# Performance work log

Measured on AMD Instinct MI355X. Metric: run time of the kernel, lower is better.

Reference implementation:

```python
import jax, jax.numpy as jnp
import numpy as np

N = 50000   # nodes
E = 800000  # edges
C = 64      # num_channels
EPS = 1e-5


def setup_inputs() -> dict:
    key = jax.random.key(0)
    ks = jax.random.split(key, 12)
    x = jax.random.normal(ks[0], (N, C), dtype=jnp.float32)
    vec = jax.random.normal(ks[1], (N, 3, C), dtype=jnp.float32)
    senders = jax.random.randint(ks[2], (E,), 0, N, dtype=jnp.int32)
    receivers = jax.random.randint(ks[3], (E,), 0, N, dtype=jnp.int32)
    interaction_matrices = jax.random.normal(ks[4], (E, 3, 3), dtype=jnp.float32)
    # learned parameters
    ln_scale = jnp.ones((C,), dtype=jnp.float32)
    ln_bias = jnp.zeros((C,), dtype=jnp.float32)
    vln_weight = jnp.ones((C,), dtype=jnp.float32)  # VecLayerNorm weight (norm_type='none' -> identity norm, channel scale)
    w1 = jax.random.normal(ks[5], (C, 2 * C), dtype=jnp.float32) / np.sqrt(C)
    b1 = jnp.zeros((2 * C,), dtype=jnp.float32)
    w2 = jax.random.normal(ks[6], (2 * C, C), dtype=jnp.float32) / np.sqrt(2 * C)
    b2 = jnp.zeros((C,), dtype=jnp.float32)
    return {
        "x": x, "vec": vec, "senders": senders, "receivers": receivers,
        "interaction_matrices": interaction_matrices,
        "ln_scale": ln_scale, "ln_bias": ln_bias, "vln_weight": vln_weight,
        "w1": w1, "b1": b1, "w2": w2, "b2": b2,
    }


def reference(x, vec, senders, receivers, interaction_matrices,
              ln_scale, ln_bias, vln_weight, w1, b1, w2, b2):
    # LayerNorm(eps=1e-5) over channel dim
    mean = jnp.mean(x, axis=-1, keepdims=True)
    var = jnp.var(x, axis=-1, keepdims=True)
    x_norm = (x - mean) * jax.lax.rsqrt(var + EPS) * ln_scale + ln_bias
    # VecLayerNorm with norm_type='none': identity norm, learned per-channel weight
    vec_norm = vec * vln_weight  # [N, 3, C]
    # MLP: Dense(2C) -> silu -> Dense(C)
    p = jax.nn.silu(x_norm @ w1 + b1) @ w2 + b2  # [N, C]
    # gather to edges
    p_i = p[receivers]            # [E, C]
    p_j = p[senders]              # [E, C]
    vec_i = vec_norm[receivers]   # [E, 3, C]
    vec_j = vec_norm[senders]     # [E, 3, C]
    source_dipole = p_j[:, None, :] * vec_j                              # [E, 3, C]
    field_at_i = jnp.einsum('eij,ejc->eic', interaction_matrices, source_dipole)  # [E, 3, C]
    dEnergy = jnp.sum(p_i[:, None, :] * vec_i * field_at_i, axis=1)      # [E, C]
    dx = jax.ops.segment_sum(dEnergy, receivers, num_segments=x.shape[0])  # [N, C]
    return dx
```

## Files before the change

### kernel.cpp

```cpp
#include <hip/hip_runtime.h>

#define C 64
#define EPS 1e-5f
#define BUCK_CAP 1536
#define OVF_CAP 65536
#define SMASK 0x03ffffffu

typedef __attribute__((ext_vector_type(8))) short bf16x8;
typedef __attribute__((ext_vector_type(4))) float f32x4;

static __device__ __forceinline__ unsigned int f2bf(float f) {
  unsigned int x = __float_as_uint(f);
  return (x + 0x7fffu + ((x >> 16) & 1u)) >> 16;
}
static __device__ __forceinline__ float bflo2f(unsigned int p) {
  return __uint_as_float(p << 16);
}
static __device__ __forceinline__ float bfhi2f(unsigned int p) {
  return __uint_as_float(p & 0xffff0000u);
}

__global__ __launch_bounds__(256) void prep_weights(
    const float* __restrict__ w1, const float* __restrict__ w2,
    unsigned short* __restrict__ w1T, unsigned short* __restrict__ w2T) {
  int idx = blockIdx.x * 256 + threadIdx.x;
  if (idx < 2 * C * C) {
    int k = idx >> 6, c = idx & 63;
    w1T[idx] = (unsigned short)f2bf(w1[c * 2 * C + k]);
  } else if (idx < 4 * C * C) {
    int j = idx - 2 * C * C;
    int c = j >> 7, k = j & 127;
    w2T[j] = (unsigned short)f2bf(w2[k * C + c]);
  }
}

__global__ __launch_bounds__(256) void bin_kernel(
    const int* __restrict__ recv, const int* __restrict__ send,
    uint2* __restrict__ region, int* __restrict__ bucketCnt,
    int* __restrict__ ovfList, int* __restrict__ ovfCnt,
    int n_edges, int nbuck) {
  __shared__ int hist[1024];
  int t = threadIdx.x;
  for (int i = t; i < 1024; i += 256) hist[i] = 0;
  __syncthreads();

  int base = blockIdx.x * 4096;
  int myrecv[16], mysend[16];
#pragma unroll 16
  for (int j = 0; j < 16; j++) {
    int e = base + j * 256 + t;
    if (e < n_edges) {
      int r = recv[e];
      myrecv[j] = r;
      mysend[j] = send[e];
      atomicAdd(&hist[r >> 6], 1);
    } else {
      myrecv[j] = -1;
      mysend[j] = 0;
    }
  }
  __syncthreads();

  for (int i = t; i < nbuck; i += 256) {
    int c = hist[i];
    hist[i] = (c > 0) ? atomicAdd(&bucketCnt[i], c) : 0;
  }
  __syncthreads();

#pragma unroll 16
  for (int j = 0; j < 16; j++) {
    int r = myrecv[j];
    if (r >= 0) {
      int e = base + j * 256 + t;
      int b = r >> 6;
      int pos = atomicAdd(&hist[b], 1);
      if (pos < BUCK_CAP) {
        uint2 rec;
        rec.x = (unsigned)mysend[j] | ((unsigned)(r & 63) << 26);
        rec.y = (unsigned)e;
        region[(size_t)b * BUCK_CAP + pos] = rec;
      } else {
        int o = atomicAdd(ovfCnt, 1);
        if (o < OVF_CAP) ovfList[o] = e;
      }
    }
  }
}

__global__ __launch_bounds__(256) void sort_kernel(
    uint2* __restrict__ region, const int* __restrict__ bucketCnt,
    int* __restrict__ nodeBeg, int* __restrict__ nodeEnd, int n_nodes) {
  __shared__ uint2 buf[BUCK_CAP];
  __shared__ int hist[64];
  __shared__ int off[64];
  int b = blockIdx.x;
  int t = threadIdx.x;
  int cnt = bucketCnt[b];
  if (cnt > BUCK_CAP) cnt = BUCK_CAP;
  uint2* reg = region + (size_t)b * BUCK_CAP;

  if (t < 64) hist[t] = 0;
  __syncthreads();
  for (int i = t; i < cnt; i += 256) {
    uint2 r = reg[i];
    buf[i] = r;
    atomicAdd(&hist[r.x >> 26], 1);
  }
  __syncthreads();
  if (t == 0) {
    int run = 0;
#pragma unroll
    for (int j = 0; j < 64; j++) { off[j] = run; run += hist[j]; }
  }
  __syncthreads();
  for (int i = t; i < cnt; i += 256) {
    uint2 r = buf[i];
    int pos = atomicAdd(&off[r.x >> 26], 1);
    reg[pos] = r;
  }
  __syncthreads();
  if (t < 64) {
    int node = b * 64 + t;
    if (node < n_nodes) {
      int end = off[t];
      nodeBeg[node] = b * BUCK_CAP + (end - hist[t]);
      nodeEnd[node] = b * BUCK_CAP + end;
    }
  }
}

__global__ __launch_bounds__(256, 4) void node_kernel(
    const float* __restrict__ x, const float* __restrict__ vec,
    const float* __restrict__ ln_scale, const float* __restrict__ ln_bias,
    const float* __restrict__ vln_w,
    const unsigned short* __restrict__ w1T, const float* __restrict__ b1,
    const unsigned short* __restrict__ w2T, const float* __restrict__ b2,
    uint2* __restrict__ D16, int n_nodes) {
  __shared__ unsigned short An[64 * 72];
  __shared__ unsigned short Ss[64 * 136];

  const int t = threadIdx.x;
  const int lane = t & 63;
  const int wave = t >> 6;
  const int l15 = lane & 15;
  const int q = lane >> 4;

  {
    int rowl = t >> 2;
    int part = t & 3;
    int node = blockIdx.x * 64 + rowl;
    int nc = node < n_nodes ? node : n_nodes - 1;
    const float* xp = x + (size_t)nc * C + part * 16;
    float xv[16];
    float s = 0.f;
#pragma unroll
    for (int i = 0; i < 4; i++) {
      float4 v = *(const float4*)(xp + i * 4);
      xv[i * 4 + 0] = v.x; xv[i * 4 + 1] = v.y;
      xv[i * 4 + 2] = v.z; xv[i * 4 + 3] = v.w;
      s += v.x + v.y + v.z + v.w;
    }
    s += __shfl_xor(s, 1);
    s += __shfl_xor(s, 2);
    float mean = s * (1.f / C);
    float vs = 0.f;
#pragma unroll
    for (int i = 0; i < 16; i++) {
      float d = xv[i] - mean;
      vs += d * d;
    }
    vs += __shfl_xor(vs, 1);
    vs += __shfl_xor(vs, 2);
    float rs = rsqrtf(vs * (1.f / C) + EPS);
    float ls[16], lb[16];
#pragma unroll
    for (int i = 0; i < 4; i++) {
      float4 a = *(const float4*)(ln_scale + part * 16 + i * 4);
      float4 b = *(const float4*)(ln_bias + part * 16 + i * 4);
      ls[i * 4 + 0] = a.x; ls[i * 4 + 1] = a.y; ls[i * 4 + 2] = a.z; ls[i * 4 + 3] = a.w;
      lb[i * 4 + 0] = b.x; lb[i * 4 + 1] = b.y; lb[i * 4 + 2] = b.z; lb[i * 4 + 3] = b.w;
    }
    unsigned int bp[8];
#pragma unroll
    for (int i = 0; i < 8; i++) {
      float e0 = (xv[2 * i] - mean) * rs * ls[2 * i] + lb[2 * i];
      float e1 = (xv[2 * i + 1] - mean) * rs * ls[2 * i + 1] + lb[2 * i + 1];
      bp[i] = f2bf(e0) | (f2bf(e1) << 16);
    }
    uint4* dst = (uint4*)(An + rowl * 72 + part * 16);
    uint4 p0 = {bp[0], bp[1], bp[2], bp[3]};
    uint4 p1 = {bp[4], bp[5], bp[6], bp[7]};
    dst[0] = p0;
    dst[1] = p1;
  }
  __syncthreads();

  const int Mbase = wave * 16;

  bf16x8 a0 = *(const bf16x8*)(An + (Mbase + l15) * 72 + q * 8);
  bf16x8 a1 = *(const bf16x8*)(An + (Mbase + l15) * 72 + 32 + q * 8);
  f32x4 acc1[8];
#pragma unroll
  for (int nt = 0; nt < 8; nt++) {
    const unsigned short* wb = w1T + (nt * 16 + l15) * 64 + q * 8;
    bf16x8 b0 = *(const bf16x8*)(wb);
    bf16x8 b1f = *(const bf16x8*)(wb + 32);
    f32x4 z = {0.f, 0.f, 0.f, 0.f};
    z = __builtin_amdgcn_mfma_f32_16x16x32_bf16(a0, b0, z, 0, 0, 0);
    z = __builtin_amdgcn_mfma_f32_16x16x32_bf16(a1, b1f, z, 0, 0, 0);
    acc1[nt] = z;
  }
#pragma unroll
  for (int nt = 0; nt < 8; nt++) {
    float bb = b1[nt * 16 + l15];
#pragma unroll
    for (int r = 0; r < 4; r++) {
      float h = acc1[nt][r] + bb;
      float sg = h / (1.f + __expf(-h));
      Ss[(Mbase + q * 4 + r) * 136 + nt * 16 + l15] = (unsigned short)f2bf(sg);
    }
  }
  __syncthreads();

  bf16x8 a2[4];
#pragma unroll
  for (int kt = 0; kt < 4; kt++)
    a2[kt] = *(const bf16x8*)(Ss + (Mbase + l15) * 136 + kt * 32 + q * 8);
  f32x4 acc2[4];
#pragma unroll
  for (int nt = 0; nt < 4; nt++) {
    f32x4 z = {0.f, 0.f, 0.f, 0.f};
#pragma unroll
    for (int kt = 0; kt < 4; kt++) {
      bf16x8 b = *(const bf16x8*)(w2T + (nt * 16 + l15) * 128 + kt * 32 + q * 8);
      z = __builtin_amdgcn_mfma_f32_16x16x32_bf16(a2[kt], b, z, 0, 0, 0);
    }
    acc2[nt] = z;
  }

#pragma unroll
  for (int nt = 0; nt < 4; nt++) {
    int cc = nt * 16 + l15;
    float bb = b2[cc];
    float vw = vln_w[cc];
#pragma unroll
    for (int r = 0; r < 4; r++) {
      int rl = Mbase + q * 4 + r;
      int nn = blockIdx.x * 64 + rl;
      if (nn < n_nodes) {
        float p = (acc2[nt][r] + bb) * vw;
        const float* vp = vec + (size_t)nn * (3 * C) + cc;
        float v0 = vp[0], v1 = vp[C], v2 = vp[2 * C];
        uint2 u;
        u.x = f2bf(p * v0) | (f2bf(p * v1) << 16);
        u.y = f2bf(p * v2);
        D16[(size_t)nn * C + cc] = u;
      }
    }
  }
}

__global__ __launch_bounds__(256) void accum_node(
    const uint2* __restrict__ region, const int* __restrict__ nodeBeg,
    const int* __restrict__ nodeEnd, const float* __restrict__ Mmat,
    const uint2* __restrict__ D2, float* __restrict__ dx, int n_nodes) {
  int wid = threadIdx.x >> 6;
  int lane = threadIdx.x & 63;
  int n = blockIdx.x * 4 + wid;
  if (n >= n_nodes) return;

  int beg = __builtin_amdgcn_readfirstlane(nodeBeg[n]);
  int end = __builtin_amdgcn_readfirstlane(nodeEnd[n]);

  uint2 dr = D2[(size_t)n * C + lane];
  float r0 = bflo2f(dr.x), r1 = bfhi2f(dr.x), r2 = bflo2f(dr.y);
  float acc = 0.f;

  if (beg < end) {
    const int last = end - 1;
    uint2 svA, svB, svC, svD, svE, svF;
    float mA[9], mB[9], mC[9], mD[9], mE[9], mF[9];

#define LOADSLOT(SV, MM, IDX)                                                \
  {                                                                          \
    uint2 rec_ = region[(IDX)];                                              \
    SV = D2[(size_t)(rec_.x & SMASK) * C + lane];                            \
    const float* Mp_ =                                                       \
        Mmat + (size_t)__builtin_amdgcn_readfirstlane((int)rec_.y) * 9;      \
    _Pragma("unroll") for (int j_ = 0; j_ < 9; j_++) MM[j_] = Mp_[j_];       \
  }

#define COMPUTE(SV, MM)                                                      \
  {                                                                          \
    float a0 = bflo2f(SV.x), a1 = bfhi2f(SV.x), a2 = bflo2f(SV.y);           \
    float f0 = MM[0] * a0 + MM[1] * a1 + MM[2] * a2;                         \
    float f1 = MM[3] * a0 + MM[4] * a1 + MM[5] * a2;                         \
    float f2 = MM[6] * a0 + MM[7] * a1 + MM[8] * a2;                         \
    acc += r0 * f0 + r1 * f1 + r2 * f2;                                      \
  }

    int i1 = (beg + 1 > last) ? last : beg + 1;
    int i2 = (beg + 2 > last) ? last : beg + 2;
    int i3 = (beg + 3 > last) ? last : beg + 3;
    int i4 = (beg + 4 > last) ? last : beg + 4;
    int i5 = (beg + 5 > last) ? last : beg + 5;
    LOADSLOT(svA, mA, beg)
    LOADSLOT(svB, mB, i1)
    LOADSLOT(svC, mC, i2)
    LOADSLOT(svD, mD, i3)
    LOADSLOT(svE, mE, i4)
    LOADSLOT(svF, mF, i5)

    for (int e = beg; e <= last; e += 6) {
#define STAGE(K, SV, MM)                                                     \
  if (e + (K) <= last) {                                                     \
    COMPUTE(SV, MM)                                                          \
    int nx = e + (K) + 6;                                                    \
    if (nx <= last) LOADSLOT(SV, MM, nx)                                     \
  }
      STAGE(0, svA, mA)
      STAGE(1, svB, mB)
      STAGE(2, svC, mC)
      STAGE(3, svD, mD)
      STAGE(4, svE, mE)
      STAGE(5, svF, mF)
#undef STAGE
    }
#undef LOADSLOT
#undef COMPUTE
  }
  dx[(size_t)n * C + lane] = acc;
}

__global__ __launch_bounds__(256) void fixup_kernel(
    const int* __restrict__ ovfList, const int* __restrict__ ovfCnt,
    const int* __restrict__ senders, const int* __restrict__ receivers,
    const float* __restrict__ Mmat, const uint2* __restrict__ D2,
    float* __restrict__ dx) {
  int nov = *ovfCnt;
  if (nov > OVF_CAP) nov = OVF_CAP;
  int lane = threadIdx.x & 63;
  for (int idx = blockIdx.x * 4 + (threadIdx.x >> 6); idx < nov;
       idx += gridDim.x * 4) {
    int e = ovfList[idx];
    int s = senders[e];
    int r = receivers[e];
    uint2 sv = D2[(size_t)s * C + lane];
    uint2 rv = D2[(size_t)r * C + lane];
    const float* M = Mmat + (size_t)e * 9;
    float a0 = bflo2f(sv.x), a1 = bfhi2f(sv.x), a2 = bflo2f(sv.y);
    float c0 = bflo2f(rv.x), c1 = bfhi2f(rv.x), c2 = bflo2f(rv.y);
    float f0 = M[0] * a0 + M[1] * a1 + M[2] * a2;
    float f1 = M[3] * a0 + M[4] * a1 + M[5] * a2;
    float f2 = M[6] * a0 + M[7] * a1 + M[8] * a2;
    float dE = c0 * f0 + c1 * f1 + c2 * f2;
    atomicAdd(dx + (size_t)r * C + lane, dE);
  }
}

extern "C" void kernel_launch(void* const* d_in, const int* in_sizes, int n_in,
                              void* d_out, int out_size, void* d_ws, size_t ws_size,
                              hipStream_t stream) {
  const float* x        = (const float*)d_in[0];
  const float* vec      = (const float*)d_in[1];
  const int*   senders  = (const int*)d_in[2];
  const int*   receivers= (const int*)d_in[3];
  const float* Mmat     = (const float*)d_in[4];
  const float* ln_scale = (const float*)d_in[5];
  const float* ln_bias  = (const float*)d_in[6];
  const float* vln_w    = (const float*)d_in[7];
  const float* w1       = (const float*)d_in[8];
  const float* b1       = (const float*)d_in[9];
  const float* w2       = (const float*)d_in[10];
  const float* b2       = (const float*)d_in[11];
  float* dx = (float*)d_out;

  int n_nodes = in_sizes[0] / C;
  int n_edges = in_sizes[2];
  int nbuck = (n_nodes + 63) >> 6;

  unsigned short* w1T = (unsigned short*)d_ws;
  unsigned short* w2T = w1T + 2 * C * C;
  uint2* D16 = (uint2*)((char*)d_ws + 32768);
  char* p = (char*)d_ws + 32768 + (size_t)n_nodes * C * sizeof(uint2);
  p = (char*)(((size_t)p + 255) & ~(size_t)255);
  int* cnts    = (int*)p;  p += (1024 + 1) * 4;
  p = (char*)(((size_t)p + 255) & ~(size_t)255);
  uint2* region = (uint2*)p;  p += (size_t)nbuck * BUCK_CAP * 8;
  int* nodeBeg = (int*)p;     p += (size_t)n_nodes * 4;
  int* nodeEnd = (int*)p;     p += (size_t)n_nodes * 4;
  int* ovfList = (int*)p;
  int* bucketCnt = cnts;
  int* ovfCnt = cnts + 1024;

  prep_weights<<<64, 256, 0, stream>>>(w1, w2, w1T, w2T);

  hipMemsetAsync(cnts, 0, (1024 + 1) * sizeof(int), stream);
  bin_kernel<<<(n_edges + 4095) / 4096, 256, 0, stream>>>(
      receivers, senders, region, bucketCnt, ovfList, ovfCnt, n_edges, nbuck);

  sort_kernel<<<nbuck, 256, 0, stream>>>(
      region, bucketCnt, nodeBeg, nodeEnd, n_nodes);

  node_kernel<<<(n_nodes + 63) / 64, 256, 0, stream>>>(
      x, vec, ln_scale, ln_bias, vln_w, w1T, b1, w2T, b2, D16, n_nodes);

  accum_node<<<(n_nodes + 3) / 4, 256, 0, stream>>>(
      region, nodeBeg, nodeEnd, Mmat, D16, dx, n_nodes);

  fixup_kernel<<<128, 256, 0, stream>>>(
      ovfList, ovfCnt, senders, receivers, Mmat, D16, dx);
}
```

Measured before the change: 269.4 us.

## Pack sorted edge records with bf16 interaction matrices into compact contiguous array

The sort kernel now gathers each edge's 3x3 interaction matrix, converts it to bf16 and writes it next to the sender index in a densely packed 24-byte record, using a new bucket prefix-scan so buckets sit contiguously. The accumulation kernel then streams these records sequentially instead of doing a random 36-byte gather of the fp32 matrix per edge. Its prefetch depth also grows from 6 to 8 slots. The cost is an extra scan launch, the gather moving into the sort kernel, more registers, and lower matrix precision from bf16 rounding.

```diff
diff --git a/kernel.cpp b/kernel.cpp
--- a/kernel.cpp
+++ b/kernel.cpp
@@ -87,9 +87,32 @@
   }
 }
 
+__global__ __launch_bounds__(1024) void scan_buckets(
+    const int* __restrict__ bucketCnt, int* __restrict__ bucketBase,
+    int nbuck) {
+  __shared__ int part[1024];
+  int t = threadIdx.x;
+  int v = 0;
+  if (t < nbuck) {
+    v = bucketCnt[t];
+    if (v > BUCK_CAP) v = BUCK_CAP;
+  }
+  part[t] = v;
+  __syncthreads();
+  for (int d = 1; d < 1024; d <<= 1) {
+    int u = (t >= d) ? part[t - d] : 0;
+    __syncthreads();
+    part[t] += u;
+    __syncthreads();
+  }
+  bucketBase[t] = part[t] - v;
+}
+
 __global__ __launch_bounds__(256) void sort_kernel(
-    uint2* __restrict__ region, const int* __restrict__ bucketCnt,
-    int* __restrict__ nodeBeg, int* __restrict__ nodeEnd, int n_nodes) {
+    const uint2* __restrict__ region, const int* __restrict__ bucketCnt,
+    const int* __restrict__ bucketBase, const float* __restrict__ Mmat,
+    uint2* __restrict__ fat, int* __restrict__ nodeBeg,
+    int* __restrict__ nodeEnd, int n_nodes) {
   __shared__ uint2 buf[BUCK_CAP];
   __shared__ int hist[64];
   __shared__ int off[64];
@@ -97,7 +120,8 @@
   int t = threadIdx.x;
   int cnt = bucketCnt[b];
   if (cnt > BUCK_CAP) cnt = BUCK_CAP;
-  uint2* reg = region + (size_t)b * BUCK_CAP;
+  const uint2* reg = region + (size_t)b * BUCK_CAP;
+  int base = bucketBase[b];
 
   if (t < 64) hist[t] = 0;
   __syncthreads();
@@ -116,15 +140,28 @@
   for (int i = t; i < cnt; i += 256) {
     uint2 r = buf[i];
     int pos = atomicAdd(&off[r.x >> 26], 1);
-    reg[pos] = r;
+    const float* Mp = Mmat + (size_t)r.y * 9;
+    float m0 = Mp[0], m1 = Mp[1], m2 = Mp[2], m3 = Mp[3], m4 = Mp[4];
+    float m5 = Mp[5], m6 = Mp[6], m7 = Mp[7], m8 = Mp[8];
+    size_t fi = (size_t)(base + pos) * 3;
+    uint2 wa, wb, wc;
+    wa.x = r.x;
+    wa.y = f2bf(m0) | (f2bf(m1) << 16);
+    wb.x = f2bf(m2) | (f2bf(m3) << 16);
+    wb.y = f2bf(m4) | (f2bf(m5) << 16);
+    wc.x = f2bf(m6) | (f2bf(m7) << 16);
+    wc.y = f2bf(m8);
+    fat[fi] = wa;
+    fat[fi + 1] = wb;
+    fat[fi + 2] = wc;
   }
   __syncthreads();
   if (t < 64) {
     int node = b * 64 + t;
     if (node < n_nodes) {
       int end = off[t];
-      nodeBeg[node] = b * BUCK_CAP + (end - hist[t]);
-      nodeEnd[node] = b * BUCK_CAP + end;
+      nodeBeg[node] = base + (end - hist[t]);
+      nodeEnd[node] = base + end;
     }
   }
 }
@@ -261,9 +298,9 @@
 }
 
 __global__ __launch_bounds__(256) void accum_node(
-    const uint2* __restrict__ region, const int* __restrict__ nodeBeg,
-    const int* __restrict__ nodeEnd, const float* __restrict__ Mmat,
-    const uint2* __restrict__ D2, float* __restrict__ dx, int n_nodes) {
+    const uint2* __restrict__ fat, const int* __restrict__ nodeBeg,
+    const int* __restrict__ nodeEnd, const uint2* __restrict__ D2,
+    float* __restrict__ dx, int n_nodes) {
   int wid = threadIdx.x >> 6;
   int lane = threadIdx.x & 63;
   int n = blockIdx.x * 4 + wid;
@@ -278,24 +315,29 @@
 
   if (beg < end) {
     const int last = end - 1;
-    uint2 svA, svB, svC, svD, svE, svF;
-    float mA[9], mB[9], mC[9], mD[9], mE[9], mF[9];
-
-#define LOADSLOT(SV, MM, IDX)                                                \
+    uint2 svA, svB, svC, svD, svE, svF, svG, svH;
+    uint2 fA[3], fB[3], fC[3], fD[3], fE[3], fF[3], fG[3], fH[3];
+
+#define LOADSLOT(SV, FM, IDX)                                                \
   {                                                                          \
-    uint2 rec_ = region[(IDX)];                                              \
-    SV = D2[(size_t)(rec_.x & SMASK) * C + lane];                            \
-    const float* Mp_ =                                                       \
-        Mmat + (size_t)__builtin_amdgcn_readfirstlane((int)rec_.y) * 9;      \
-    _Pragma("unroll") for (int j_ = 0; j_ < 9; j_++) MM[j_] = Mp_[j_];       \
-  }
-
-#define COMPUTE(SV, MM)                                                      \
+    size_t fi_ = (size_t)(IDX) * 3;                                          \
+    FM[0] = fat[fi_];                                                        \
+    FM[1] = fat[fi_ + 1];                                                    \
+    FM[2] = fat[fi_ + 2];                                                    \
+    SV = D2[(size_t)(FM[0].x & SMASK) * C + lane];                           \
+  }
+
+#define COMPUTE(SV, FM)                                                      \
   {                                                                          \
     float a0 = bflo2f(SV.x), a1 = bfhi2f(SV.x), a2 = bflo2f(SV.y);           \
-    float f0 = MM[0] * a0 + MM[1] * a1 + MM[2] * a2;                         \
-    float f1 = MM[3] * a0 + MM[4] * a1 + MM[5] * a2;                         \
-    float f2 = MM[6] * a0 + MM[7] * a1 + MM[8] * a2;                         \
+    float m00 = bflo2f(FM[0].y), m01 = bfhi2f(FM[0].y);                      \
+    float m02 = bflo2f(FM[1].x), m10 = bfhi2f(FM[1].x);                      \
+    float m11 = bflo2f(FM[1].y), m12 = bfhi2f(FM[1].y);                      \
+    float m20 = bflo2f(FM[2].x), m21 = bfhi2f(FM[2].x);                      \
+    float m22 = bflo2f(FM[2].y);                                             \
+    float f0 = m00 * a0 + m01 * a1 + m02 * a2;                               \
+    float f1 = m10 * a0 + m11 * a1 + m12 * a2;                               \
+    float f2 = m20 * a0 + m21 * a1 + m22 * a2;                               \
     acc += r0 * f0 + r1 * f1 + r2 * f2;                                      \
   }
 
@@ -304,26 +346,32 @@
     int i3 = (beg + 3 > last) ? last : beg + 3;
     int i4 = (beg + 4 > last) ? last : beg + 4;
     int i5 = (beg + 5 > last) ? last : beg + 5;
-    LOADSLOT(svA, mA, beg)
-    LOADSLOT(svB, mB, i1)
-    LOADSLOT(svC, mC, i2)
-    LOADSLOT(svD, mD, i3)
-    LOADSLOT(svE, mE, i4)
-    LOADSLOT(svF, mF, i5)
-
-    for (int e = beg; e <= last; e += 6) {
-#define STAGE(K, SV, MM)                                                     \
+    int i6 = (beg + 6 > last) ? last : beg + 6;
+    int i7 = (beg + 7 > last) ? last : beg + 7;
+    LOADSLOT(svA, fA, beg)
+    LOADSLOT(svB, fB, i1)
+    LOADSLOT(svC, fC, i2)
+    LOADSLOT(svD, fD, i3)
+    LOADSLOT(svE, fE, i4)
+    LOADSLOT(svF, fF, i5)
+    LOADSLOT(svG, fG, i6)
+    LOADSLOT(svH, fH, i7)
+
+    for (int e = beg; e <= last; e += 8) {
+#define STAGE(K, SV, FM)                                                     \
   if (e + (K) <= last) {                                                     \
-    COMPUTE(SV, MM)                                                          \
-    int nx = e + (K) + 6;                                                    \
-    if (nx <= last) LOADSLOT(SV, MM, nx)                                     \
-  }
-      STAGE(0, svA, mA)
-      STAGE(1, svB, mB)
-      STAGE(2, svC, mC)
-      STAGE(3, svD, mD)
-      STAGE(4, svE, mE)
-      STAGE(5, svF, mF)
+    COMPUTE(SV, FM)                                                          \
+    int nx = e + (K) + 8;                                                    \
+    if (nx <= last) LOADSLOT(SV, FM, nx)                                     \
+  }
+      STAGE(0, svA, fA)
+      STAGE(1, svB, fB)
+      STAGE(2, svC, fC)
+      STAGE(3, svD, fD)
+      STAGE(4, svE, fE)
+      STAGE(5, svF, fF)
+      STAGE(6, svG, fG)
+      STAGE(7, svH, fH)
 #undef STAGE
     }
 #undef LOADSLOT
@@ -384,12 +432,15 @@
   uint2* D16 = (uint2*)((char*)d_ws + 32768);
   char* p = (char*)d_ws + 32768 + (size_t)n_nodes * C * sizeof(uint2);
   p = (char*)(((size_t)p + 255) & ~(size_t)255);
-  int* cnts    = (int*)p;  p += (1024 + 1) * 4;
+  int* cnts       = (int*)p;  p += (1024 + 1) * 4;
+  p = (char*)(((size_t)p + 255) & ~(size_t)255);
+  int* bucketBase = (int*)p;  p += 1024 * 4;
   p = (char*)(((size_t)p + 255) & ~(size_t)255);
   uint2* region = (uint2*)p;  p += (size_t)nbuck * BUCK_CAP * 8;
-  int* nodeBeg = (int*)p;     p += (size_t)n_nodes * 4;
-  int* nodeEnd = (int*)p;     p += (size_t)n_nodes * 4;
-  int* ovfList = (int*)p;
+  uint2* fat    = (uint2*)p;  p += (size_t)n_edges * 24;
+  int* nodeBeg  = (int*)p;    p += (size_t)n_nodes * 4;
+  int* nodeEnd  = (int*)p;    p += (size_t)n_nodes * 4;
+  int* ovfList  = (int*)p;
   int* bucketCnt = cnts;
   int* ovfCnt = cnts + 1024;
 
@@ -399,14 +450,16 @@
   bin_kernel<<<(n_edges + 4095) / 4096, 256, 0, stream>>>(
       receivers, senders, region, bucketCnt, ovfList, ovfCnt, n_edges, nbuck);
 
+  scan_buckets<<<1, 1024, 0, stream>>>(bucketCnt, bucketBase, nbuck);
+
   sort_kernel<<<nbuck, 256, 0, stream>>>(
-      region, bucketCnt, nodeBeg, nodeEnd, n_nodes);
+      region, bucketCnt, bucketBase, Mmat, fat, nodeBeg, nodeEnd, n_nodes);
 
   node_kernel<<<(n_nodes + 63) / 64, 256, 0, stream>>>(
       x, vec, ln_scale, ln_bias, vln_w, w1T, b1, w2T, b2, D16, n_nodes);
 
   accum_node<<<(n_nodes + 3) / 4, 256, 0, stream>>>(
-      region, nodeBeg, nodeEnd, Mmat, D16, dx, n_nodes);
+      fat, nodeBeg, nodeEnd, D16, dx, n_nodes);
 
   fixup_kernel<<<128, 256, 0, stream>>>(
       ovfList, ovfCnt, senders, receivers, Mmat, D16, dx);
```

New measurement: 269.8 us. Within noise of the previous version (+0.1%).
